# Optimization experiments

Hardware: AMD Instinct MI355X
Metric: run time of the kernel (lower is better)

Reference implementation:

```python
import jax, jax.numpy as jnp
import numpy as np


def setup_inputs() -> dict:
    key = jax.random.key(0)
    ks = jax.random.split(key, 5)
    B, I, H = 16384, 1024, 1024
    return {
        "input": jax.random.normal(ks[0], (B, I), dtype=jnp.float32),
        "h_prev": jax.random.normal(ks[1], (B, H), dtype=jnp.float32),
        "c_prev": jax.random.normal(ks[2], (B, H), dtype=jnp.float32),
        "W_ih": jax.random.normal(ks[3], (4 * H, I), dtype=jnp.float32),
        "W_hh": jax.random.normal(ks[4], (4 * H, H), dtype=jnp.float32),
        "b_ih": jnp.zeros((4 * H,), dtype=jnp.float32),
        "b_hh": jnp.zeros((4 * H,), dtype=jnp.float32),
    }


def reference(input, h_prev, c_prev, W_ih, W_hh, b_ih, b_hh):
    H = h_prev.shape[1]
    gi = input @ W_ih.T + b_ih          # [B, 4H]
    gh = h_prev @ W_hh.T + b_hh         # [B, 4H]
    g = gi + gh
    # chunk order in source: input_gate, forget_gate, candidate, output_gate
    i_g = jax.nn.sigmoid(g[:, 0 * H:1 * H])
    f_g = jax.nn.sigmoid(g[:, 1 * H:2 * H])
    cand = jnp.tanh(g[:, 2 * H:3 * H])
    o_g = jax.nn.sigmoid(g[:, 3 * H:4 * H])
    c_new = c_prev * f_g + i_g * cand
    h_new = jnp.tanh(c_new) * o_g
    return (h_new, c_new)
```

## Files before the change

### kernel.cpp

```cpp
#include <hip/hip_runtime.h>
#include <cstdint>
#include <cstddef>


typedef _Float16 half8 __attribute__((ext_vector_type(8)));
typedef float f32x4 __attribute__((ext_vector_type(4)));

__device__ __forceinline__ float sigmoidf_(float x) { return 1.0f / (1.0f + __expf(-x)); }
__device__ __forceinline__ float tanh_fast(float x) { return 2.0f / (1.0f + __expf(-2.0f * x)) - 1.0f; }

__device__ __forceinline__ void gld16(const void* g, void* lds) {
    __builtin_amdgcn_global_load_lds((const __attribute__((address_space(1))) uint32_t*)g,
                                     (__attribute__((address_space(3))) uint32_t*)lds, 16, 0, 0);
}

__global__ __launch_bounds__(256)
void convert_to_f16(const float* __restrict__ X, const float* __restrict__ H,
                    const float* __restrict__ Wih, const float* __restrict__ Whh,
                    _Float16* __restrict__ ws, long nX, long nW)
{
    long e = ((long)blockIdx.x * 256 + threadIdx.x) * 8;
    long total = 2 * nX + 2 * nW;
    if (e >= total) return;
    const float* src; long off;
    if (e < nX)              { src = X;   off = e; }
    else if (e < 2 * nX)     { src = H;   off = e - nX; }
    else if (e < 2 * nX + nW){ src = Wih; off = e - 2 * nX; }
    else                     { src = Whh; off = e - 2 * nX - nW; }
    float4 a = *(const float4*)(src + off);
    float4 b = *(const float4*)(src + off + 4);
    half8 h;
    h[0]=(_Float16)a.x; h[1]=(_Float16)a.y; h[2]=(_Float16)a.z; h[3]=(_Float16)a.w;
    h[4]=(_Float16)b.x; h[5]=(_Float16)b.y; h[6]=(_Float16)b.z; h[7]=(_Float16)b.w;
    *(half8*)(ws + e) = h;
}

__global__ __launch_bounds__(512, 2)
void lstm_mfma_v3(const _Float16* __restrict__ ws,
                  const float* __restrict__ Cprev,
                  const float* __restrict__ bih, const float* __restrict__ bhh,
                  float* __restrict__ Out, int Btot, int mblocks)
{
    __shared__ alignas(16) char smem[131072];

    const long nX = (long)Btot * 1024;
    const long nW = 4096L * 1024;
    const _Float16* Xh = ws;
    const _Float16* Hh = ws + nX;
    const _Float16* Wi = ws + 2 * nX;
    const _Float16* Wh = ws + 2 * nX + nW;

    const int tid = threadIdx.x;
    const int w = tid >> 6, l = tid & 63;
    const int lr = l & 15, q = l >> 4;
    const int wm = w >> 2, wn = w & 3;

    const int nwg = gridDim.x;
    int bx = blockIdx.x;
    if ((nwg & 7) == 0) bx = (bx & 7) * (nwg >> 3) + (bx >> 3);
    const int m0   = (bx % mblocks) * 256;
    const int hblk = (bx / mblocks) * 64;

    uint32_t gA[2], gB[2], ub[2];
    #pragma unroll
    for (int j = 0; j < 2; ++j) {
        uint32_t u = (uint32_t)(j * 8192 + w * 1024);
        ub[j] = u;
        uint32_t off = u + (uint32_t)l * 16u;
        uint32_t r  = off >> 6;
        uint32_t c  = ((off >> 4) & 3u) ^ ((r >> 1) & 3u);
        gA[j] = (uint32_t)(m0 + (int)r) * 1024u + c * 8u;
        uint32_t gate = (r >> 4) & 3u;
        uint32_t hsub = (r >> 6) * 16u + (r & 15u);
        gB[j] = (gate * 1024u + (uint32_t)hblk + hsub) * 1024u + c * 8u;
    }

    const int sw = (lr >> 1) & 3;
    const int ck = (q ^ sw) * 16;
    const uint32_t aB0 = (uint32_t)((wm * 128 + lr) * 64 + ck);
    const uint32_t bB0 = (uint32_t)((wn * 64  + lr) * 64 + ck);

    f32x4 acc[8][4];
    #pragma unroll
    for (int i = 0; i < 8; ++i)
        #pragma unroll
        for (int j = 0; j < 4; ++j)
            acc[i][j] = (f32x4){0.f, 0.f, 0.f, 0.f};

    auto stage = [&](int ts, int sb) {
        const _Float16* Ap = (ts < 32) ? Xh : Hh;
        const _Float16* Bp = (ts < 32) ? Wi : Wh;
        const uint32_t k0 = (uint32_t)(ts & 31) * 32u;
        char* bA = smem + sb * 16384;
        char* bB = smem + 65536 + sb * 16384;
        gld16(Ap + gA[0] + k0, bA + ub[0]);
        gld16(Ap + gA[1] + k0, bA + ub[1]);
        gld16(Bp + gB[0] + k0, bB + ub[0]);
        gld16(Bp + gB[1] + k0, bB + ub[1]);
    };

    stage(0, 0); stage(1, 1); stage(2, 2);
    asm volatile("s_waitcnt vmcnt(8)" ::: "memory");
    __builtin_amdgcn_s_barrier();

    #pragma unroll 1
    for (int t = 0; t < 64; ++t) {
        const int b = t & 3;
        const char* sA = smem + b * 16384;
        const char* sB = smem + 65536 + b * 16384;

        int ts = t + 3; if (ts > 63) ts = 63;
        stage(ts, (t + 3) & 3);

        half8 bf[4], af[4];
        #pragma unroll
        for (int nt = 0; nt < 4; ++nt) bf[nt] = *(const half8*)(sB + bB0 + nt * 1024);
        #pragma unroll
        for (int mt = 0; mt < 4; ++mt) af[mt] = *(const half8*)(sA + aB0 + mt * 1024);
        __builtin_amdgcn_s_barrier();
        asm volatile("s_waitcnt lgkmcnt(0)" ::: "memory");
        __builtin_amdgcn_sched_barrier(0);
        __builtin_amdgcn_s_setprio(1);
        #pragma unroll
        for (int mt = 0; mt < 4; ++mt)
            #pragma unroll
            for (int nt = 0; nt < 4; ++nt)
                acc[mt][nt] = __builtin_amdgcn_mfma_f32_16x16x32_f16(af[mt], bf[nt], acc[mt][nt], 0, 0, 0);
        __builtin_amdgcn_s_setprio(0);
        __builtin_amdgcn_sched_barrier(0);
        __builtin_amdgcn_s_barrier();

        half8 ag[4];
        #pragma unroll
        for (int mt = 0; mt < 4; ++mt) ag[mt] = *(const half8*)(sA + aB0 + (mt + 4) * 1024);
        __builtin_amdgcn_s_barrier();
        asm volatile("s_waitcnt lgkmcnt(0)" ::: "memory");
        __builtin_amdgcn_sched_barrier(0);
        __builtin_amdgcn_s_setprio(1);
        #pragma unroll
        for (int mt = 0; mt < 4; ++mt)
            #pragma unroll
            for (int nt = 0; nt < 4; ++nt)
                acc[mt + 4][nt] = __builtin_amdgcn_mfma_f32_16x16x32_f16(ag[mt], bf[nt], acc[mt + 4][nt], 0, 0, 0);
        __builtin_amdgcn_s_setprio(0);
        asm volatile("s_waitcnt vmcnt(8)" ::: "memory");
        __builtin_amdgcn_sched_barrier(0);
        __builtin_amdgcn_s_barrier();
    }
    asm volatile("s_waitcnt vmcnt(0)" ::: "memory");

    const int h = hblk + wn * 16 + lr;
    float bs[4];
    #pragma unroll
    for (int g = 0; g < 4; ++g) bs[g] = bih[g * 1024 + h] + bhh[g * 1024 + h];
    const long c_off = (long)Btot * 1024;
    const int mbase = m0 + wm * 128 + q * 4;

    #pragma unroll
    for (int mt = 0; mt < 8; ++mt) {
        #pragma unroll
        for (int r = 0; r < 4; ++r) {
            const int m = mbase + mt * 16 + r;
            const long idx = (long)m * 1024 + h;
            float gi = acc[mt][0][r] + bs[0];
            float gf = acc[mt][1][r] + bs[1];
            float gc = acc[mt][2][r] + bs[2];
            float go = acc[mt][3][r] + bs[3];
            float ig = sigmoidf_(gi), fg = sigmoidf_(gf);
            float cd = tanh_fast(gc), og = sigmoidf_(go);
            float c_new = Cprev[idx] * fg + ig * cd;
            Out[idx]         = tanh_fast(c_new) * og;
            Out[c_off + idx] = c_new;
        }
    }
}

__global__ __launch_bounds__(256, 2)
void lstm_mfma_f16_fb(const float* __restrict__ X, const float* __restrict__ Hprev,
                      const float* __restrict__ Cprev,
                      const float* __restrict__ Wih, const float* __restrict__ Whh,
                      const float* __restrict__ bih, const float* __restrict__ bhh,
                      float* __restrict__ Out, int Btot, int mblocks)
{
    __shared__ alignas(16) _Float16 As[128][40];
    __shared__ alignas(16) _Float16 Bs[256][40];
    const int tid = threadIdx.x;
    const int w = tid >> 6, lane = tid & 63, lr = lane & 15, q = lane >> 4;
    const int bx = blockIdx.x, mblk = bx % mblocks, nblk = bx / mblocks;
    const int m0 = mblk * 128, hblk = nblk * 64;
    const int sr = tid >> 1, sc = tid & 1;
    f32x4 acc[8][4];
    #pragma unroll
    for (int mt = 0; mt < 8; ++mt)
        #pragma unroll
        for (int g = 0; g < 4; ++g) acc[mt][g] = (f32x4){0.f,0.f,0.f,0.f};
    float4 pa[4], pb0[4], pb1[4];
    const int rb1 = sr + 128;
    const size_t wrow0 = (size_t)((sr >> 6) * 1024 + hblk + (sr & 63)) * 1024;
    const size_t wrow1 = (size_t)((rb1 >> 6) * 1024 + hblk + (rb1 & 63)) * 1024;
    const size_t arow  = (size_t)(m0 + sr) * 1024;
    auto stage_load = [&](int tile) {
        const int phase = tile >> 5;
        const int k0 = (tile & 31) * 32 + sc * 16;
        const float* Ap = phase ? Hprev : X;
        const float* Wp = phase ? Whh : Wih;
        const float4* ap = (const float4*)(Ap + arow + k0);
        const float4* b0 = (const float4*)(Wp + wrow0 + k0);
        const float4* b1 = (const float4*)(Wp + wrow1 + k0);
        #pragma unroll
        for (int i = 0; i < 4; ++i) { pa[i] = ap[i]; pb0[i] = b0[i]; pb1[i] = b1[i]; }
    };
    auto pack8 = [](float4 a, float4 b) {
        half8 h;
        h[0]=(_Float16)a.x; h[1]=(_Float16)a.y; h[2]=(_Float16)a.z; h[3]=(_Float16)a.w;
        h[4]=(_Float16)b.x; h[5]=(_Float16)b.y; h[6]=(_Float16)b.z; h[7]=(_Float16)b.w;
        return h;
    };
    stage_load(0);
    for (int tile = 0; tile < 64; ++tile) {
        __syncthreads();
        *(half8*)&As[sr][sc*16]        = pack8(pa[0], pa[1]);
        *(half8*)&As[sr][sc*16+8]      = pack8(pa[2], pa[3]);
        *(half8*)&Bs[sr][sc*16]        = pack8(pb0[0], pb0[1]);
        *(half8*)&Bs[sr][sc*16+8]      = pack8(pb0[2], pb0[3]);
        *(half8*)&Bs[sr+128][sc*16]    = pack8(pb1[0], pb1[1]);
        *(half8*)&Bs[sr+128][sc*16+8]  = pack8(pb1[2], pb1[3]);
        __syncthreads();
        if (tile + 1 < 64) stage_load(tile + 1);
        half8 bf[4];
        #pragma unroll
        for (int g = 0; g < 4; ++g) bf[g] = *(const half8*)&Bs[g*64 + w*16 + lr][q*8];
        #pragma unroll
        for (int mt = 0; mt < 8; ++mt) {
            half8 a = *(const half8*)&As[mt*16 + lr][q*8];
            #pragma unroll
            for (int g = 0; g < 4; ++g)
                acc[mt][g] = __builtin_amdgcn_mfma_f32_16x16x32_f16(a, bf[g], acc[mt][g], 0, 0, 0);
        }
    }
    const int h = hblk + w * 16 + lr;
    float bs0 = bih[h] + bhh[h];
    float bs1 = bih[1024+h] + bhh[1024+h];
    float bs2 = bih[2048+h] + bhh[2048+h];
    float bs3 = bih[3072+h] + bhh[3072+h];
    const size_t c_off = (size_t)Btot * 1024;
    #pragma unroll
    for (int mt = 0; mt < 8; ++mt)
        #pragma unroll
        for (int r = 0; r < 4; ++r) {
            const int m = m0 + mt*16 + q*4 + r;
            const size_t idx = (size_t)m * 1024 + h;
            float gi = acc[mt][0][r]+bs0, gf = acc[mt][1][r]+bs1;
            float gc = acc[mt][2][r]+bs2, go = acc[mt][3][r]+bs3;
            float ig = sigmoidf_(gi), fg = sigmoidf_(gf);
            float cd = tanh_fast(gc), og = sigmoidf_(go);
            float c_new = Cprev[idx]*fg + ig*cd;
            Out[idx] = tanh_fast(c_new)*og;
            Out[c_off+idx] = c_new;
        }
}

extern "C" void kernel_launch(void* const* d_in, const int* in_sizes, int n_in,
                              void* d_out, int out_size, void* d_ws, size_t ws_size,
                              hipStream_t stream) {
    const float* X     = (const float*)d_in[0];
    const float* Hprev = (const float*)d_in[1];
    const float* Cprev = (const float*)d_in[2];
    const float* Wih   = (const float*)d_in[3];
    const float* Whh   = (const float*)d_in[4];
    const float* bih   = (const float*)d_in[5];
    const float* bhh   = (const float*)d_in[6];
    float* Out = (float*)d_out;

    const int Btot = in_sizes[0] / 1024;
    const long nX = (long)Btot * 1024, nW = 4096L * 1024;
    const size_t need = (size_t)(2 * nX + 2 * nW) * sizeof(_Float16);

    if (ws_size >= need && (Btot % 256) == 0) {
        _Float16* ws = (_Float16*)d_ws;
        const long total = 2 * nX + 2 * nW;
        const int cblocks = (int)((total / 8 + 255) / 256);
        hipLaunchKernelGGL(convert_to_f16, dim3(cblocks), dim3(256), 0, stream,
                           X, Hprev, Wih, Whh, ws, nX, nW);
        const int mblocks = Btot / 256;
        const int nblocks = 1024 / 64;
        hipLaunchKernelGGL(lstm_mfma_v3, dim3(mblocks * nblocks), dim3(512), 0, stream,
                           ws, Cprev, bih, bhh, Out, Btot, mblocks);
    } else {
        const int mblocks = Btot / 128;
        hipLaunchKernelGGL(lstm_mfma_f16_fb, dim3(mblocks * 16), dim3(256), 0, stream,
                           X, Hprev, Cprev, Wih, Whh, bih, bhh, Out, Btot, mblocks);
    }
}
```

Baseline: 561.9 us.

## Double-buffer LDS fragment registers to overlap next tile reads with MFMAs

Restructures the main GEMM loop into a software-pipelined form. Two register sets of A/B fragments are kept, so LDS reads for tile t+1 are issued while the MFMAs for tile t run. The explicit lgkmcnt waits and extra barriers per iteration are removed, leaving one barrier per tile and a tighter vmcnt wait. This roughly doubles fragment register usage, which could cause spills under the 512x2 launch bounds. Dropping sched_barriers and lgkmcnt waits also leaves correctness to the compiler's implicit waits.

```diff
diff --git a/kernel.cpp b/kernel.cpp
--- a/kernel.cpp
+++ b/kernel.cpp
@@ -36,7 +36,7 @@
 }
 
 __global__ __launch_bounds__(512, 2)
-void lstm_mfma_v3(const _Float16* __restrict__ ws,
+void lstm_mfma_v4(const _Float16* __restrict__ ws,
                   const float* __restrict__ Cprev,
                   const float* __restrict__ bih, const float* __restrict__ bhh,
                   float* __restrict__ Out, int Btot, int mblocks)
@@ -99,54 +99,56 @@
         gld16(Bp + gB[1] + k0, bB + ub[1]);
     };
 
+    half8 afA[4], bfA[4], agA[4];
+    half8 afB[4], bfB[4], agB[4];
+
     stage(0, 0); stage(1, 1); stage(2, 2);
-    asm volatile("s_waitcnt vmcnt(8)" ::: "memory");
+    asm volatile("s_waitcnt vmcnt(4)" ::: "memory");
     __builtin_amdgcn_s_barrier();
+    #pragma unroll
+    for (int i = 0; i < 4; ++i) bfA[i] = *(const half8*)(smem + 65536 + bB0 + i * 1024);
+    #pragma unroll
+    for (int i = 0; i < 4; ++i) afA[i] = *(const half8*)(smem + aB0 + i * 1024);
+    #pragma unroll
+    for (int i = 0; i < 4; ++i) agA[i] = *(const half8*)(smem + aB0 + (i + 4) * 1024);
+
+#define TILE_HALF(T, CAF, CBF, CAG, NAF, NBF, NAG)                                   \
+    {                                                                                \
+        const int t_ = (T);                                                          \
+        int ts_ = t_ + 3; if (ts_ > 63) ts_ = 63;                                    \
+        stage(ts_, (t_ + 3) & 3);                                                    \
+        const char* sAn = smem + ((t_ + 1) & 3) * 16384;                             \
+        const char* sBn = smem + 65536 + ((t_ + 1) & 3) * 16384;                     \
+        _Pragma("unroll")                                                            \
+        for (int i = 0; i < 4; ++i) NBF[i] = *(const half8*)(sBn + bB0 + i * 1024);  \
+        __builtin_amdgcn_s_setprio(1);                                               \
+        _Pragma("unroll")                                                            \
+        for (int mt = 0; mt < 4; ++mt)                                               \
+            _Pragma("unroll")                                                        \
+            for (int nt = 0; nt < 4; ++nt)                                           \
+                acc[mt][nt] = __builtin_amdgcn_mfma_f32_16x16x32_f16(CAF[mt], CBF[nt], acc[mt][nt], 0, 0, 0); \
+        __builtin_amdgcn_s_setprio(0);                                               \
+        _Pragma("unroll")                                                            \
+        for (int i = 0; i < 4; ++i) NAF[i] = *(const half8*)(sAn + aB0 + i * 1024);  \
+        __builtin_amdgcn_s_setprio(1);                                               \
+        _Pragma("unroll")                                                            \
+        for (int mt = 0; mt < 4; ++mt)                                               \
+            _Pragma("unroll")                                                        \
+            for (int nt = 0; nt < 4; ++nt)                                           \
+                acc[mt + 4][nt] = __builtin_amdgcn_mfma_f32_16x16x32_f16(CAG[mt], CBF[nt], acc[mt + 4][nt], 0, 0, 0); \
+        __builtin_amdgcn_s_setprio(0);                                               \
+        _Pragma("unroll")                                                            \
+        for (int i = 0; i < 4; ++i) NAG[i] = *(const half8*)(sAn + aB0 + (i + 4) * 1024); \
+        asm volatile("s_waitcnt vmcnt(4)" ::: "memory");                             \
+        __builtin_amdgcn_s_barrier();                                                \
+    }
 
     #pragma unroll 1
-    for (int t = 0; t < 64; ++t) {
-        const int b = t & 3;
-        const char* sA = smem + b * 16384;
-        const char* sB = smem + 65536 + b * 16384;
-
-        int ts = t + 3; if (ts > 63) ts = 63;
-        stage(ts, (t + 3) & 3);
-
-        half8 bf[4], af[4];
-        #pragma unroll
-        for (int nt = 0; nt < 4; ++nt) bf[nt] = *(const half8*)(sB + bB0 + nt * 1024);
-        #pragma unroll
-        for (int mt = 0; mt < 4; ++mt) af[mt] = *(const half8*)(sA + aB0 + mt * 1024);
-        __builtin_amdgcn_s_barrier();
-        asm volatile("s_waitcnt lgkmcnt(0)" ::: "memory");
-        __builtin_amdgcn_sched_barrier(0);
-        __builtin_amdgcn_s_setprio(1);
-        #pragma unroll
-        for (int mt = 0; mt < 4; ++mt)
-            #pragma unroll
-            for (int nt = 0; nt < 4; ++nt)
-                acc[mt][nt] = __builtin_amdgcn_mfma_f32_16x16x32_f16(af[mt], bf[nt], acc[mt][nt], 0, 0, 0);
-        __builtin_amdgcn_s_setprio(0);
-        __builtin_amdgcn_sched_barrier(0);
-        __builtin_amdgcn_s_barrier();
-
-        half8 ag[4];
-        #pragma unroll
-        for (int mt = 0; mt < 4; ++mt) ag[mt] = *(const half8*)(sA + aB0 + (mt + 4) * 1024);
-        __builtin_amdgcn_s_barrier();
-        asm volatile("s_waitcnt lgkmcnt(0)" ::: "memory");
-        __builtin_amdgcn_sched_barrier(0);
-        __builtin_amdgcn_s_setprio(1);
-        #pragma unroll
-        for (int mt = 0; mt < 4; ++mt)
-            #pragma unroll
-            for (int nt = 0; nt < 4; ++nt)
-                acc[mt + 4][nt] = __builtin_amdgcn_mfma_f32_16x16x32_f16(ag[mt], bf[nt], acc[mt + 4][nt], 0, 0, 0);
-        __builtin_amdgcn_s_setprio(0);
-        asm volatile("s_waitcnt vmcnt(8)" ::: "memory");
-        __builtin_amdgcn_sched_barrier(0);
-        __builtin_amdgcn_s_barrier();
-    }
+    for (int p = 0; p < 32; ++p) {
+        TILE_HALF(2 * p,     afA, bfA, agA, afB, bfB, agB)
+        TILE_HALF(2 * p + 1, afB, bfB, agB, afA, bfA, agA)
+    }
+#undef TILE_HALF
     asm volatile("s_waitcnt vmcnt(0)" ::: "memory");
 
     const int h = hblk + wn * 16 + lr;
@@ -284,7 +286,7 @@
                            X, Hprev, Wih, Whh, ws, nX, nW);
         const int mblocks = Btot / 256;
         const int nblocks = 1024 / 64;
-        hipLaunchKernelGGL(lstm_mfma_v3, dim3(mblocks * nblocks), dim3(512), 0, stream,
+        hipLaunchKernelGGL(lstm_mfma_v4, dim3(mblocks * nblocks), dim3(512), 0, stream,
                            ws, Cprev, bih, bhh, Out, Btot, mblocks);
     } else {
         const int mblocks = Btot / 128;
```

New measurement: 555.5 us. No clear change (-1.1%).
